# Kernel optimization log

Measured on AMD Instinct MI355X. Metric: run time of the kernel, lower is better.

## Reference

```python
import jax, jax.numpy as jnp
import numpy as np

DISTANCES = [1, 2]
ANGLES_DEG = [0.0, 45.0, 90.0, 135.0]
LEVELS = 32
FEATURES = ["contrast", "homogeneity", "energy", "correlation"]

# skimage graycomatrix offsets: row = r + round(sin(a)*d), col = c + round(cos(a)*d)
OFFSETS = [(int(np.round(np.sin(np.deg2rad(a)) * d)), int(np.round(np.cos(np.deg2rad(a)) * d)))
           for d in DISTANCES for a in ANGLES_DEG]


def _quantize(images, levels):
    # RGB -> gray, [-1,1] -> [0,1] -> integer gray levels (uint8 floor cast in original)
    gray = images.mean(axis=1)                                  # [B,H,W]
    g = jnp.clip((gray + 1.0) * 0.5 * (levels - 1), 0.0, levels - 1)
    return g.astype(jnp.int32)


def _glcm(g, dr, dc, levels):
    # symmetric, normed co-occurrence matrix for one (distance, angle) offset
    B, H, W = g.shape
    r0, r1 = max(0, -dr), H - max(0, dr)
    c0, c1 = max(0, -dc), W - max(0, dc)
    i = g[:, r0:r1, c0:c1]
    j = g[:, r0 + dr:r1 + dr, c0 + dc:c1 + dc]
    idx = (i * levels + j).reshape(B, -1)                        # [B, n_pairs]
    hist = jax.vmap(lambda ix: jnp.zeros(levels * levels, jnp.float32).at[ix].add(1.0))(idx)
    P = hist.reshape(B, levels, levels)
    P = P + jnp.swapaxes(P, 1, 2)                                # symmetric
    return P / jnp.sum(P, axis=(1, 2), keepdims=True)            # normed


def _prop(P, feat):
    # graycoprops formulas; P: [B, L, L]
    L = P.shape[-1]
    I = jnp.arange(L, dtype=jnp.float32)[:, None]                # [L,1]
    J = jnp.arange(L, dtype=jnp.float32)[None, :]                # [1,L]
    if feat == "contrast":
        return jnp.sum(P * (I - J) ** 2, axis=(1, 2))
    if feat == "homogeneity":
        return jnp.sum(P / (1.0 + (I - J) ** 2), axis=(1, 2))
    if feat == "energy":
        return jnp.sqrt(jnp.sum(P * P, axis=(1, 2)))
    if feat == "correlation":
        mu_i = jnp.sum(I * P, axis=(1, 2))                       # [B]
        mu_j = jnp.sum(J * P, axis=(1, 2))
        di = I[None] - mu_i[:, None, None]
        dj = J[None] - mu_j[:, None, None]
        std_i = jnp.sqrt(jnp.sum(P * di * di, axis=(1, 2)))
        std_j = jnp.sqrt(jnp.sum(P * dj * dj, axis=(1, 2)))
        cov = jnp.sum(P * di * dj, axis=(1, 2))
        denom = std_i * std_j
        return jnp.where(denom > 1e-15, cov / jnp.where(denom > 1e-15, denom, 1.0), 1.0)
    raise ValueError(feat)


def reference(images):
    g = _quantize(images, LEVELS)
    # accumulate feature values over all (distance, angle) offsets, then mean
    acc = {f: 0.0 for f in FEATURES}
    for (dr, dc) in OFFSETS:
        P = _glcm(g, dr, dc, LEVELS)
        for f in FEATURES:
            acc[f] = acc[f] + _prop(P, f)
    n = float(len(OFFSETS))
    return jnp.stack([acc[f] / n for f in FEATURES], axis=0)     # [n_features, B]


def setup_inputs() -> dict:
    key = jax.random.key(0)
    images = jax.random.normal(key, (64, 3, 512, 512), dtype=jnp.float32)
    return {"images": images}
```

## Files before the change

### kernel.cpp

```cpp
#include <hip/hip_runtime.h>

typedef unsigned int uint;

#define HW (512 * 512)
#define NIMG 64
#define NUQ 6
#define RSTRIDE 528
#define RINGROWS 16
#define RINGBYTES (RINGROWS * RSTRIDE)
#define RINGA 32768
#define RINGB (32768 + RINGBYTES)
#define SMEMB (32768 + 2 * RINGBYTES)

__device__ __constant__ float UOFF_W[NUQ] = {1.f, 2.f, 1.f, 2.f, 1.f, 1.f};
__device__ __constant__ float NPAIRS[NUQ] = {
    512.f * 511.f, 511.f * 511.f, 511.f * 512.f,
    511.f * 511.f, 512.f * 510.f, 510.f * 512.f};

__device__ __forceinline__ uint q1f(float a, float b, float c) {
    float t = fmaf(a + b + c, 5.1666665f, 15.5f);
    t = fminf(fmaxf(t, 0.0f), 31.0f);
    return (uint)t;
}

__global__ __launch_bounds__(256) void glcm_fused(
    const float* __restrict__ in, uint* __restrict__ wire) {
    __shared__ __align__(16) unsigned char smem[SMEMB];
    const int tid = threadIdx.x;
    const int b = blockIdx.x >> 3;
    const int sp = blockIdx.x & 7;
    const int rsA = sp * 32;
    const int rsB = sp * 32 + 256;
    const float* ib = in + (size_t)b * (3 * HW);
    const int lrow = tid >> 6;
    const int lcol = (tid & 63) << 3;

    {
        uint4 z = make_uint4(0, 0, 0, 0);
        #pragma unroll
        for (int q = 0; q < 8; ++q)
            *(uint4*)(smem + tid * 16 + q * 4096) = z;
    }
    __syncthreads();

    auto issueL = [&](int rs, int c, float4& A0, float4& B0, float4& A1,
                      float4& B1, float4& A2, float4& B2) {
        int R = rs - 2 + 4 * c + lrow;
        int Rc = min(max(R, 0), 511);
        const float* p = ib + ((size_t)Rc << 9) + lcol;
        A0 = *(const float4*)(p);
        B0 = *(const float4*)(p + 4);
        A1 = *(const float4*)(p + HW);
        B1 = *(const float4*)(p + HW + 4);
        A2 = *(const float4*)(p + 2 * HW);
        B2 = *(const float4*)(p + 2 * HW + 4);
    };

    auto quantW = [&](int rs, int ringo, int c, const float4& A0, const float4& B0,
                      const float4& A1, const float4& B1, const float4& A2,
                      const float4& B2) {
        int R = rs - 2 + 4 * c + lrow;
        if (R >= 0 && R <= 511) {
            uint q0 = (q1f(A0.x, A1.x, A2.x) << 2)
                    | (q1f(A0.y, A1.y, A2.y) << 10)
                    | (q1f(A0.z, A1.z, A2.z) << 18)
                    | (q1f(A0.w, A1.w, A2.w) << 26);
            uint q1_ = (q1f(B0.x, B1.x, B2.x) << 2)
                     | (q1f(B0.y, B1.y, B2.y) << 10)
                     | (q1f(B0.z, B1.z, B2.z) << 18)
                     | (q1f(B0.w, B1.w, B2.w) << 26);
            unsigned char* rw = smem + ringo + ((R + 2) & 15) * RSTRIDE;
            *(uint2*)(rw + lcol) = make_uint2(q0, q1_);
            if ((tid & 63) == 63)
                *(uint4*)(rw + 512) = make_uint4(0x80808080u, 0x80808080u,
                                                 0x80808080u, 0x80808080u);
        }
    };

    auto histC = [&](int rs, int ringo, int h) {
        const unsigned char* ring = smem + ringo;
        #pragma unroll
        for (int rr = 0; rr < 2; ++rr) {
            const int R = rs + 4 * h + 2 * rr + (tid >> 7);
            const int dq = tid & 127;
            const uint* rowL   = (const uint*)(ring + ((R + 2) & 15) * RSTRIDE);
            const uint* rowLm  = (const uint*)(ring + ((R + 1) & 15) * RSTRIDE);
            const uint* rowLp  = (const uint*)(ring + ((R + 3) & 15) * RSTRIDE);
            const uint* rowLpp = (const uint*)(ring + ((R + 4) & 15) * RSTRIDE);
            uint A  = rowL[dq],  A1 = rowL[dq + 1];
            uint Bm = rowLp[dq], B1 = rowLp[dq + 1];
            uint Cm = rowLm[dq], C1 = rowLm[dq + 1];
            uint D  = rowLpp[dq];

            auto pp4 = [&](uint IW, uint JW, int tagoff, uint inc) {
                uint jm = (JW >> 2) & 0x1F1F1F1Fu;
                uint im = (IW >> 2) & 0x1F1F1F1Fu;
                uint s  = (jm + im + (im << 1)) & 0x1F1F1F1Fu;
                uint J2 = (s << 2) | (JW & 0x80808080u);
                uint a0 = __builtin_amdgcn_perm(IW, J2, 0x0C0C0400u);
                uint a1 = __builtin_amdgcn_perm(IW, J2, 0x0C0C0501u);
                uint a2 = __builtin_amdgcn_perm(IW, J2, 0x0C0C0602u);
                uint a3 = __builtin_amdgcn_perm(IW, J2, 0x0C0C0703u);
                atomicAdd((uint*)(smem + tagoff + a0), inc);
                atomicAdd((uint*)(smem + tagoff + a1), inc);
                atomicAdd((uint*)(smem + tagoff + a2), inc);
                atomicAdd((uint*)(smem + tagoff + a3), inc);
            };
            if (R < 512) pp4(A, __builtin_amdgcn_alignbyte(A1, A, 1), 0, 1u);
            if (R < 511) pp4(A, __builtin_amdgcn_alignbyte(B1, Bm, 1), 256, 1u);
            if (R < 511) pp4(A, Bm, 512, 1u);
            if (R >= 1 && R < 512)
                pp4(A, __builtin_amdgcn_alignbyte(C1, Cm, 1), 0, 65536u);
            if (R < 512) pp4(A, __builtin_amdgcn_alignbyte(A1, A, 2), 256, 65536u);
            if (R < 510) pp4(A, D, 512, 65536u);
        }
    };

    float4 a0, b0, a1, b1, a2, b2;
    for (int i = 0; i < 10; ++i) {
        if (i <= 8) issueL(rsA, i, a0, b0, a1, b1, a2, b2);
        if (i >= 2) histC(rsB, RINGB, i - 2);
        if (i <= 8) quantW(rsA, RINGA, i, a0, b0, a1, b1, a2, b2);
        __syncthreads();
        if (i <= 8) issueL(rsB, i, a0, b0, a1, b1, a2, b2);
        if (i >= 2) histC(rsA, RINGA, i - 2);
        if (i <= 8) quantW(rsB, RINGB, i, a0, b0, a1, b1, a2, b2);
        __syncthreads();
    }

    uint* hw = wire + (size_t)blockIdx.x * 3072;
    const uint* hist = (const uint*)smem;
    #pragma unroll
    for (int qq = 0; qq < 12; ++qq) {
        int o = tid + qq * 256;
        int tg = o >> 10, ij = o & 1023;
        int i2 = ij >> 5, j = ij & 31;
        hw[o] = hist[(i2 << 8) | (tg << 6) | ((j + 3 * i2) & 31)];
    }
}

__global__ __launch_bounds__(256) void feature_out_kernel(
    const uint* __restrict__ wire, float* __restrict__ out) {
    const int b = blockIdx.x;
    __shared__ uint cnt[NUQ][1024];
    __shared__ float fred[NUQ][4];
    const int tid = threadIdx.x, wid = tid >> 6, lane = tid & 63;

    for (int u = wid; u < NUQ; u += 4) {
        const int tg = (u < 3) ? u : u - 3;
        const int sh = (u < 3) ? 0 : 16;
        const uint* p = wire + (size_t)b * (8 * 3072) + tg * 1024;
        for (int ij = lane; ij < 1024; ij += 64) {
            uint acc = 0;
            #pragma unroll
            for (int st = 0; st < 8; ++st)
                acc += (p[(size_t)st * 3072 + ij] >> sh) & 0xFFFFu;
            cnt[u][ij] = acc;
        }
    }
    __syncthreads();

    for (int u = wid; u < NUQ; u += 4) {
        const float inv_total = 1.0f / (2.0f * NPAIRS[u]);
        float c_sum = 0, h_sum = 0, e_sum = 0, m1 = 0, m2 = 0, m12 = 0;
        for (int k = lane; k < 1024; k += 64) {
            int i = k >> 5, j = k & 31;
            float sym = (float)(cnt[u][k] + cnt[u][(j << 5) | i]);
            float P = sym * inv_total;
            float d = (float)(i - j);
            float d2 = d * d;
            float fi = (float)i, fj = (float)j;
            c_sum += P * d2;
            h_sum += P / (1.0f + d2);
            e_sum += P * P;
            m1 += P * fi; m2 += P * fi * fi; m12 += P * fi * fj;
        }
        #pragma unroll
        for (int sft = 32; sft > 0; sft >>= 1) {
            c_sum += __shfl_down(c_sum, sft);
            h_sum += __shfl_down(h_sum, sft);
            e_sum += __shfl_down(e_sum, sft);
            m1 += __shfl_down(m1, sft);
            m2 += __shfl_down(m2, sft);
            m12 += __shfl_down(m12, sft);
        }
        if (lane == 0) {
            float mu = m1, var = m2 - mu * mu, cov = m12 - mu * mu;
            float corr = (var > 1e-15f) ? cov / var : 1.0f;
            fred[u][0] = c_sum; fred[u][1] = h_sum;
            fred[u][2] = sqrtf(e_sum); fred[u][3] = corr;
        }
    }
    __syncthreads();
    if (tid < 4) {
        float acc = 0.f;
        #pragma unroll
        for (int u = 0; u < NUQ; ++u) acc += UOFF_W[u] * fred[u][tid];
        out[tid * NIMG + b] = acc * 0.125f;
    }
}

extern "C" void kernel_launch(void* const* d_in, const int* in_sizes, int n_in,
                              void* d_out, int out_size, void* d_ws, size_t ws_size,
                              hipStream_t stream) {
    const float* images = (const float*)d_in[0];
    float* out = (float*)d_out;
    uint* wire = (uint*)d_ws;

    glcm_fused<<<NIMG * 8, 256, 0, stream>>>(images, wire);
    feature_out_kernel<<<NIMG, 256, 0, stream>>>(wire, out);
}
```

Before: 74.04 us.

## Replace dual-ring interleaved pipeline with single contiguous 64-row strip ring

Each block now processes one contiguous 64-row strip through a single 16-row shared ring, instead of two 32-row strips interleaved across two rings. This halves ring shared memory and the number of barriers per chunk, and drops halo rows that were loaded and quantized twice at the strip boundaries. In exchange it loses the interleaving of one strip's loads with the other strip's histogram work. Ring indices are made relative to the strip start, and redundant bounds checks are removed.

```diff
diff --git a/kernel.cpp b/kernel.cpp
--- a/kernel.cpp
+++ b/kernel.cpp
@@ -6,11 +6,8 @@
 #define NIMG 64
 #define NUQ 6
 #define RSTRIDE 528
-#define RINGROWS 16
-#define RINGBYTES (RINGROWS * RSTRIDE)
-#define RINGA 32768
-#define RINGB (32768 + RINGBYTES)
-#define SMEMB (32768 + 2 * RINGBYTES)
+#define RINGB 32768
+#define SMEMB (32768 + 16 * RSTRIDE)
 
 __device__ __constant__ float UOFF_W[NUQ] = {1.f, 2.f, 1.f, 2.f, 1.f, 1.f};
 __device__ __constant__ float NPAIRS[NUQ] = {
@@ -29,8 +26,7 @@
     const int tid = threadIdx.x;
     const int b = blockIdx.x >> 3;
     const int sp = blockIdx.x & 7;
-    const int rsA = sp * 32;
-    const int rsB = sp * 32 + 256;
+    const int rs = sp * 64;
     const float* ib = in + (size_t)b * (3 * HW);
     const int lrow = tid >> 6;
     const int lcol = (tid & 63) << 3;
@@ -43,8 +39,9 @@
     }
     __syncthreads();
 
-    auto issueL = [&](int rs, int c, float4& A0, float4& B0, float4& A1,
-                      float4& B1, float4& A2, float4& B2) {
+    float4 A0, B0, A1, B1, A2, B2;
+
+    auto issueL = [&](int c) {
         int R = rs - 2 + 4 * c + lrow;
         int Rc = min(max(R, 0), 511);
         const float* p = ib + ((size_t)Rc << 9) + lcol;
@@ -56,9 +53,7 @@
         B2 = *(const float4*)(p + 2 * HW + 4);
     };
 
-    auto quantW = [&](int rs, int ringo, int c, const float4& A0, const float4& B0,
-                      const float4& A1, const float4& B1, const float4& A2,
-                      const float4& B2) {
+    auto quantW = [&](int c) {
         int R = rs - 2 + 4 * c + lrow;
         if (R >= 0 && R <= 511) {
             uint q0 = (q1f(A0.x, A1.x, A2.x) << 2)
@@ -69,7 +64,7 @@
                      | (q1f(B0.y, B1.y, B2.y) << 10)
                      | (q1f(B0.z, B1.z, B2.z) << 18)
                      | (q1f(B0.w, B1.w, B2.w) << 26);
-            unsigned char* rw = smem + ringo + ((R + 2) & 15) * RSTRIDE;
+            unsigned char* rw = smem + RINGB + ((R - rs + 2) & 15) * RSTRIDE;
             *(uint2*)(rw + lcol) = make_uint2(q0, q1_);
             if ((tid & 63) == 63)
                 *(uint4*)(rw + 512) = make_uint4(0x80808080u, 0x80808080u,
@@ -77,16 +72,17 @@
         }
     };
 
-    auto histC = [&](int rs, int ringo, int h) {
-        const unsigned char* ring = smem + ringo;
+    auto histC = [&](int h) {
         #pragma unroll
         for (int rr = 0; rr < 2; ++rr) {
             const int R = rs + 4 * h + 2 * rr + (tid >> 7);
+            const int v = R - rs + 2;
             const int dq = tid & 127;
-            const uint* rowL   = (const uint*)(ring + ((R + 2) & 15) * RSTRIDE);
-            const uint* rowLm  = (const uint*)(ring + ((R + 1) & 15) * RSTRIDE);
-            const uint* rowLp  = (const uint*)(ring + ((R + 3) & 15) * RSTRIDE);
-            const uint* rowLpp = (const uint*)(ring + ((R + 4) & 15) * RSTRIDE);
+            const unsigned char* ring = smem + RINGB;
+            const uint* rowL   = (const uint*)(ring + ((v)     & 15) * RSTRIDE);
+            const uint* rowLm  = (const uint*)(ring + ((v - 1) & 15) * RSTRIDE);
+            const uint* rowLp  = (const uint*)(ring + ((v + 1) & 15) * RSTRIDE);
+            const uint* rowLpp = (const uint*)(ring + ((v + 2) & 15) * RSTRIDE);
             uint A  = rowL[dq],  A1 = rowL[dq + 1];
             uint Bm = rowLp[dq], B1 = rowLp[dq + 1];
             uint Cm = rowLm[dq], C1 = rowLm[dq + 1];
@@ -106,25 +102,22 @@
                 atomicAdd((uint*)(smem + tagoff + a2), inc);
                 atomicAdd((uint*)(smem + tagoff + a3), inc);
             };
-            if (R < 512) pp4(A, __builtin_amdgcn_alignbyte(A1, A, 1), 0, 1u);
-            if (R < 511) pp4(A, __builtin_amdgcn_alignbyte(B1, Bm, 1), 256, 1u);
-            if (R < 511) pp4(A, Bm, 512, 1u);
-            if (R >= 1 && R < 512)
+            pp4(A, __builtin_amdgcn_alignbyte(A1, A, 1), 0, 1u);
+            if (R < 511) {
+                pp4(A, __builtin_amdgcn_alignbyte(B1, Bm, 1), 256, 1u);
+                pp4(A, Bm, 512, 1u);
+            }
+            if (R >= 1)
                 pp4(A, __builtin_amdgcn_alignbyte(C1, Cm, 1), 0, 65536u);
-            if (R < 512) pp4(A, __builtin_amdgcn_alignbyte(A1, A, 2), 256, 65536u);
+            pp4(A, __builtin_amdgcn_alignbyte(A1, A, 2), 256, 65536u);
             if (R < 510) pp4(A, D, 512, 65536u);
         }
     };
 
-    float4 a0, b0, a1, b1, a2, b2;
-    for (int i = 0; i < 10; ++i) {
-        if (i <= 8) issueL(rsA, i, a0, b0, a1, b1, a2, b2);
-        if (i >= 2) histC(rsB, RINGB, i - 2);
-        if (i <= 8) quantW(rsA, RINGA, i, a0, b0, a1, b1, a2, b2);
-        __syncthreads();
-        if (i <= 8) issueL(rsB, i, a0, b0, a1, b1, a2, b2);
-        if (i >= 2) histC(rsA, RINGA, i - 2);
-        if (i <= 8) quantW(rsB, RINGB, i, a0, b0, a1, b1, a2, b2);
+    for (int c = 0; c <= 17; ++c) {
+        if (c <= 16) issueL(c);
+        if (c >= 2) histC(c - 2);
+        if (c <= 16) quantW(c);
         __syncthreads();
     }
 
```

Measured after the change: 70.78 us. 1.05x faster.
